# Optimization experiments

Measured on AMD Instinct MI355X. Metric: run time of the kernel, lower is better.

The kernel has to match this reference:

```python
import jax, jax.numpy as jnp
import numpy as np

DIM = 768
HEADS = 12
HEAD_DIM = DIM // HEADS
B, N = 8, 1024


def setup_inputs() -> dict:
    key = jax.random.key(0)
    ks = jax.random.split(key, 5)
    x = jax.random.normal(ks[0], (B, N, DIM), dtype=jnp.float32)
    shared_rel_pos = jax.random.normal(ks[1], (HEADS, N, N), dtype=jnp.float32)
    qkv_w = jax.random.normal(ks[2], (3 * DIM, DIM), dtype=jnp.float32) * (DIM ** -0.5)
    proj_w = jax.random.normal(ks[3], (DIM, DIM), dtype=jnp.float32) * (DIM ** -0.5)
    proj_b = jnp.zeros((DIM,), dtype=jnp.float32)
    return {"x": x, "shared_rel_pos": shared_rel_pos, "qkv_w": qkv_w,
            "proj_w": proj_w, "proj_b": proj_b}


def reference(x, shared_rel_pos, qkv_w, proj_w, proj_b):
    Bt, Nt, C = x.shape
    scale = HEAD_DIM ** -0.5
    # qkv: Linear(dim, 3*dim, bias=False) -> (B, N, 3, H, hd) -> (3, B, H, N, hd)
    qkv = jnp.einsum('bnc,oc->bno', x, qkv_w)
    qkv = qkv.reshape(Bt, Nt, 3, HEADS, HEAD_DIM).transpose(2, 0, 3, 1, 4)
    q, k, v = qkv[0], qkv[1], qkv[2]
    # scaled dot-product attention with shared relative-position bias
    attn = jnp.einsum('bhqd,bhkd->bhqk', q, k) * scale
    attn = attn + shared_rel_pos[None]  # broadcast over batch
    attn = jax.nn.softmax(attn, axis=-1)
    out = jnp.einsum('bhqk,bhkd->bhqd', attn, v)
    out = out.transpose(0, 2, 1, 3).reshape(Bt, Nt, C)
    return jnp.einsum('bnc,oc->bno', out, proj_w) + proj_b
```

## Files before the change

kernel.cpp:

```cpp
#include <hip/hip_runtime.h>
#include <hip/hip_bf16.h>
#include <stdint.h>

#define HEADS 12
#define HD 64
#define SEQ 1024
#define CDIM 768

typedef __attribute__((ext_vector_type(8))) short bfrag;
typedef __attribute__((ext_vector_type(4))) float facc;
typedef __attribute__((ext_vector_type(4))) _Float16 h4;

__device__ __forceinline__ ushort f2bf(float f) {
    union { float f; uint32_t u; } v; v.f = f;
    uint32_t u = v.u;
    uint32_t r = (u + 0x7FFFu + ((u >> 16) & 1u)) >> 16;
    return (ushort)r;
}
__device__ __forceinline__ ushort f2h(float f) {
    union { _Float16 h; ushort u; } c; c.h = (_Float16)f; return c.u;
}
__device__ __forceinline__ float h2f(uint32_t u16) {
    union { _Float16 h; ushort u; } c; c.u = (ushort)u16; return (float)c.h;
}

__global__ void cvt_all(const float* __restrict__ x, const float* __restrict__ qw,
                        const float* __restrict__ pw, const float* __restrict__ rel,
                        ushort* __restrict__ xd, ushort* __restrict__ qd,
                        ushort* __restrict__ pd, ushort* __restrict__ rd) {
    long i = ((long)blockIdx.x * 256 + threadIdx.x) * 4;
    if (i < 6291456) {
        float4 v = *(const float4*)(x + i);
        ushort4 o = {f2bf(v.x), f2bf(v.y), f2bf(v.z), f2bf(v.w)};
        *(ushort4*)(xd + i) = o;
    } else if (i < 8060928) {
        long j = i - 6291456;
        float4 v = *(const float4*)(qw + j);
        ushort4 o = {f2bf(v.x), f2bf(v.y), f2bf(v.z), f2bf(v.w)};
        *(ushort4*)(qd + j) = o;
    } else if (i < 8650752) {
        long j = i - 8060928;
        float4 v = *(const float4*)(pw + j);
        ushort4 o = {f2bf(v.x), f2bf(v.y), f2bf(v.z), f2bf(v.w)};
        *(ushort4*)(pd + j) = o;
    } else {
        long j = i - 8650752;
        float4 v = *(const float4*)(rel + j);
        ushort4 o = {f2h(v.x * 1.44269504f), f2h(v.y * 1.44269504f),
                     f2h(v.z * 1.44269504f), f2h(v.w * 1.44269504f)};
        *(ushort4*)(rd + j) = o;
    }
}

#define GLOAD16(gsrc, ldst) \
    __builtin_amdgcn_global_load_lds((const __attribute__((address_space(1))) uint32_t*)(gsrc), \
                                     (__attribute__((address_space(3))) uint32_t*)(ldst), 16, 0, 0)

template<int EPI>
__global__ __launch_bounds__(256) void gemm_nt(
    const ushort* __restrict__ A, const ushort* __restrict__ Bm,
    ushort* __restrict__ qb, ushort* __restrict__ kb, ushort* __restrict__ vb,
    const float* __restrict__ projb, float* __restrict__ out)
{
    __shared__ ushort As[128 * 32];
    __shared__ ushort Bs[128 * 32];
    const int t = threadIdx.x;
    const int w = t >> 6, l = t & 63;
    const int wm = w >> 1, wn = w & 1;
    const int lr = l & 15, lg = l >> 4;
    const int m0 = blockIdx.x * 128;
    const int o0 = blockIdx.y * 128;

    facc acc[4][4] = {};

    const int srow = w * 16 + (l >> 2);
    const int scol = (l & 3) * 8;
    const ushort* Ag = A + (size_t)(m0 + srow) * CDIM + scol;
    const ushort* Bg = Bm + (size_t)(o0 + srow) * CDIM + scol;

    for (int k0 = 0; k0 < CDIM; k0 += 32) {
        __syncthreads();
        GLOAD16(Ag + k0,             As + w * 512);
        GLOAD16(Ag + 64 * CDIM + k0, As + 2048 + w * 512);
        GLOAD16(Bg + k0,             Bs + w * 512);
        GLOAD16(Bg + 64 * CDIM + k0, Bs + 2048 + w * 512);
        __syncthreads();
        bfrag af[4], bf[4];
#pragma unroll
        for (int m = 0; m < 4; ++m)
            af[m] = *(const bfrag*)&As[(wm * 64 + m * 16 + lr) * 32 + lg * 8];
#pragma unroll
        for (int n = 0; n < 4; ++n)
            bf[n] = *(const bfrag*)&Bs[(wn * 64 + n * 16 + lr) * 32 + lg * 8];
#pragma unroll
        for (int m = 0; m < 4; ++m)
#pragma unroll
            for (int n = 0; n < 4; ++n)
                acc[m][n] = __builtin_amdgcn_mfma_f32_16x16x32_bf16(af[m], bf[n], acc[m][n], 0, 0, 0);
    }

    if (EPI == 0) {
        const int tsel = o0 / CDIM;
        const int h_base = (o0 % CDIM) / 64;
        ushort* dst = (tsel == 0) ? qb : ((tsel == 1) ? kb : vb);
        const float scl = (tsel == 0) ? 0.18033688f : 1.0f;
#pragma unroll
        for (int m = 0; m < 4; ++m) {
            int grow = m0 + wm * 64 + m * 16 + lg * 4;
#pragma unroll
            for (int n = 0; n < 4; ++n) {
                int h = h_base + wn;
                int d = n * 16 + lr;
#pragma unroll
                for (int r = 0; r < 4; ++r) {
                    int row = grow + r;
                    int b = row >> 10, nn = row & 1023;
                    ushort val = (tsel == 2) ? f2h(acc[m][n][r])
                                             : f2bf(acc[m][n][r] * scl);
                    dst[(((size_t)(b * HEADS + h)) * SEQ + nn) * HD + d] = val;
                }
            }
        }
    } else {
#pragma unroll
        for (int m = 0; m < 4; ++m) {
            int grow = m0 + wm * 64 + m * 16 + lg * 4;
#pragma unroll
            for (int n = 0; n < 4; ++n) {
                int o = o0 + wn * 64 + n * 16 + lr;
                float bias = projb[o];
#pragma unroll
                for (int r = 0; r < 4; ++r)
                    out[(size_t)(grow + r) * CDIM + o] = acc[m][n][r] + bias;
            }
        }
    }
}

__global__ __launch_bounds__(256, 4) void attn_kernel(
    const ushort* __restrict__ qbuf, const ushort* __restrict__ kbuf,
    const ushort* __restrict__ vbuf, const ushort* __restrict__ biash,
    ushort* __restrict__ attn_out)
{
    __shared__ ushort Ks[2][64 * 72];
    __shared__ ushort Vt[2][64 * 72];

    const int t = threadIdx.x;
    const int w = t >> 6, l = t & 63;
    const int lr = l & 15, lg = l >> 4;

    const int bid = blockIdx.x;
    const int lid = (bid & 7) * 192 + (bid >> 3);
    const int h  = lid >> 7;
    const int qt = (lid >> 3) & 15;
    const int b  = lid & 7;

    const int q0 = qt * 64;
    const size_t headoff = (size_t)(b * HEADS + h) * SEQ * HD;
    const int qrb = q0 + w * 16;

    bfrag aQ0, aQ1;
    {
        const ushort* Qp = qbuf + headoff + (size_t)(qrb + lr) * HD;
        aQ0 = *(const bfrag*)(Qp + lg * 8);
        aQ1 = *(const bfrag*)(Qp + 32 + lg * 8);
    }

    float mrun = -1e30f, lrun = 0.0f;
    facc Ov[4] = {};

    const ushort* bprow = biash + ((size_t)h * SEQ + qrb + lr) * SEQ;

    const int krow = t >> 3, kc = (t & 7) * 8;
    const int p2 = t & 31, vg_ = t >> 5;
    const ushort* kgb = kbuf + headoff + (size_t)krow * HD + kc;
    const ushort* vgb = vbuf + headoff + (size_t)(2 * p2) * HD + vg_ * 8;

    bfrag krA = *(const bfrag*)(kgb);
    bfrag krB = *(const bfrag*)(kgb + (size_t)32 * HD);
    bfrag vrA = *(const bfrag*)(vgb);
    bfrag vrB = *(const bfrag*)(vgb + HD);
    uint2 bcur[4], bnxt[4];
#pragma unroll
    for (int c = 0; c < 4; ++c)
        bcur[c] = *(const uint2*)(bprow + c * 16 + lg * 4);

    *(bfrag*)&Ks[0][krow * 72 + kc] = krA;
    *(bfrag*)&Ks[0][(krow + 32) * 72 + kc] = krB;
#pragma unroll
    for (int i = 0; i < 8; ++i) {
        uint32_t pk = (uint32_t)(uint16_t)vrA[i] | ((uint32_t)(uint16_t)vrB[i] << 16);
        *(uint32_t*)&Vt[0][(vg_ * 8 + i) * 72 + 2 * p2] = pk;
    }
    krA = *(const bfrag*)(kgb + (size_t)64 * HD);
    krB = *(const bfrag*)(kgb + (size_t)96 * HD);
    vrA = *(const bfrag*)(vgb + (size_t)64 * HD);
    vrB = *(const bfrag*)(vgb + (size_t)65 * HD);
    __syncthreads();

    for (int tt = 0; tt < 16; ++tt) {
        const int cur = tt & 1;
        const ushort* Kc = Ks[cur];
        const ushort* Vc = Vt[cur];

        facc St[4];
        h4 pf[4];
        float psum = 0.0f, pmax = -3.0e38f;
#pragma unroll
        for (int c = 0; c < 4; ++c) {
            bfrag kf0 = *(const bfrag*)&Kc[(c * 16 + lr) * 72 + lg * 8];
            bfrag kf1 = *(const bfrag*)&Kc[(c * 16 + lr) * 72 + 32 + lg * 8];
            uint2 bb = bcur[c];
            facc s;
            s[0] = h2f(bb.x & 0xffffu);
            s[1] = h2f(bb.x >> 16);
            s[2] = h2f(bb.y & 0xffffu);
            s[3] = h2f(bb.y >> 16);
            __builtin_amdgcn_s_setprio(1);
            s = __builtin_amdgcn_mfma_f32_16x16x32_bf16(kf0, aQ0, s, 0, 0, 0);
            s = __builtin_amdgcn_mfma_f32_16x16x32_bf16(kf1, aQ1, s, 0, 0, 0);
            __builtin_amdgcn_s_setprio(0);
            St[c] = s;
#pragma unroll
            for (int r = 0; r < 4; ++r) {
                float p = exp2f(s[r] - mrun);
                psum += p;
                pf[c][r] = (_Float16)p;
                pmax = fmaxf(pmax, s[r]);
            }
        }

        if (tt < 15) {
            const int kvn = (tt + 1) << 6;
#pragma unroll
            for (int c = 0; c < 4; ++c)
                bnxt[c] = *(const uint2*)(bprow + kvn + c * 16 + lg * 4);
        }

        pmax = fmaxf(pmax, __shfl_xor(pmax, 16));
        pmax = fmaxf(pmax, __shfl_xor(pmax, 32));
        if (!__all(pmax <= mrun + 11.541560f)) {
            float mnew = fmaxf(mrun, pmax);
            float al = exp2f(mrun - mnew);
            psum = 0.0f;
#pragma unroll
            for (int c = 0; c < 4; ++c)
#pragma unroll
                for (int r = 0; r < 4; ++r) {
                    float p = exp2f(St[c][r] - mnew);
                    psum += p;
                    pf[c][r] = (_Float16)p;
                }
#pragma unroll
            for (int r = 0; r < 4; ++r) {
                float a = __shfl(al, lg * 4 + r);
#pragma unroll
                for (int d = 0; d < 4; ++d) Ov[d][r] *= a;
            }
            lrun *= al;
            mrun = mnew;
        }
        psum += __shfl_xor(psum, 16);
        psum += __shfl_xor(psum, 32);
        lrun += psum;

        if (tt < 15) {
            *(bfrag*)&Ks[cur ^ 1][krow * 72 + kc] = krA;
            *(bfrag*)&Ks[cur ^ 1][(krow + 32) * 72 + kc] = krB;
#pragma unroll
            for (int i = 0; i < 8; ++i) {
                uint32_t pk = (uint32_t)(uint16_t)vrA[i] | ((uint32_t)(uint16_t)vrB[i] << 16);
                *(uint32_t*)&Vt[cur ^ 1][(vg_ * 8 + i) * 72 + 2 * p2] = pk;
            }
        }
        if (tt < 14) {
            const int kvn = (tt + 2) << 6;
            krA = *(const bfrag*)(kgb + (size_t)kvn * HD);
            krB = *(const bfrag*)(kgb + (size_t)(kvn + 32) * HD);
            vrA = *(const bfrag*)(vgb + (size_t)kvn * HD);
            vrB = *(const bfrag*)(vgb + (size_t)(kvn + 1) * HD);
        }

        __builtin_amdgcn_s_setprio(1);
#pragma unroll
        for (int d0 = 0; d0 < 4; ++d0) {
#pragma unroll
            for (int c = 0; c < 4; ++c) {
                h4 bv = *(const h4*)&Vc[(d0 * 16 + lr) * 72 + c * 16 + lg * 4];
                Ov[d0] = __builtin_amdgcn_mfma_f32_16x16x16f16(pf[c], bv, Ov[d0], 0, 0, 0);
            }
        }
        __builtin_amdgcn_s_setprio(0);

        if (tt < 15) {
            __syncthreads();
#pragma unroll
            for (int c = 0; c < 4; ++c)
                bcur[c] = bnxt[c];
        }
    }

    ushort* op = attn_out + ((size_t)b * SEQ + qrb) * CDIM + h * HD;
#pragma unroll
    for (int r = 0; r < 4; ++r) {
        float ll = __shfl(lrun, lg * 4 + r);
        float rl = 1.0f / ll;
#pragma unroll
        for (int d = 0; d < 4; ++d)
            op[(size_t)(lg * 4 + r) * CDIM + d * 16 + lr] = f2bf(Ov[d][r] * rl);
    }
}

extern "C" void kernel_launch(void* const* d_in, const int* in_sizes, int n_in,
                              void* d_out, int out_size, void* d_ws, size_t ws_size,
                              hipStream_t stream) {
    const float* x     = (const float*)d_in[0];
    const float* rel   = (const float*)d_in[1];
    const float* qkvw  = (const float*)d_in[2];
    const float* projw = (const float*)d_in[3];
    const float* projb = (const float*)d_in[4];
    float* out = (float*)d_out;

    char* ws = (char*)d_ws;
    ushort* biash = (ushort*)(ws);
    ushort* qb    = (ushort*)(ws + 25165824);
    ushort* kb    = (ushort*)(ws + 37748736);
    ushort* vb    = (ushort*)(ws + 50331648);
    ushort* attnb = (ushort*)(ws + 62914560);
    ushort* xbf   = attnb;
    ushort* wbf   = (ushort*)(ws + 75497472);
    ushort* pwbf  = (ushort*)(ws + 79036416);

    cvt_all<<<20736, 256, 0, stream>>>(x, qkvw, projw, rel, xbf, wbf, pwbf, biash);

    gemm_nt<0><<<dim3(64, 18), 256, 0, stream>>>(xbf, wbf, qb, kb, vb, nullptr, nullptr);
    attn_kernel<<<1536, 256, 0, stream>>>(qb, kb, vb, biash, attnb);
    gemm_nt<1><<<dim3(64, 6), 256, 0, stream>>>(attnb, pwbf, nullptr, nullptr, nullptr, projb, out);
}
```

Measured before the change: 164.0 us.

## Fuse bias conversion into QKV GEMM grid and widen attention blocks to 512 threads

Moves the fp32-to-fp16 conversion of the relative-position bias out of the standalone convert kernel and into extra blocks of the QKV GEMM launch, so it runs concurrently with the GEMM. Attention now uses 512-thread blocks covering 128 queries, so K/V tiles are shared by twice as many waves and each thread loads half as much K/V per tile. Softmax uses raw v_exp_f32, packed fp16 conversion with round-toward-zero, a looser rescale threshold checked via __any, and defers the cross-lane row-sum reduction to the end. These cut per-tile ALU, shuffle and load work, at the cost of higher register/LDS pressure per block and slightly different rounding.

```diff
diff --git a/kernel.cpp b/kernel.cpp
--- a/kernel.cpp
+++ b/kernel.cpp
@@ -6,10 +6,12 @@
 #define HD 64
 #define SEQ 1024
 #define CDIM 768
+#define LOG2E 1.44269504f
 
 typedef __attribute__((ext_vector_type(8))) short bfrag;
 typedef __attribute__((ext_vector_type(4))) float facc;
 typedef __attribute__((ext_vector_type(4))) _Float16 h4;
+typedef __attribute__((ext_vector_type(2))) __fp16 pk2;
 
 __device__ __forceinline__ ushort f2bf(float f) {
     union { float f; uint32_t u; } v; v.f = f;
@@ -23,11 +25,22 @@
 __device__ __forceinline__ float h2f(uint32_t u16) {
     union { _Float16 h; ushort u; } c; c.u = (ushort)u16; return (float)c.h;
 }
+__device__ __forceinline__ h4 pack4h(float p0, float p1, float p2, float p3) {
+    union { h4 v4; pk2 v2[2]; } u;
+    u.v2[0] = __builtin_amdgcn_cvt_pkrtz(p0, p1);
+    u.v2[1] = __builtin_amdgcn_cvt_pkrtz(p2, p3);
+    return u.v4;
+}
+__device__ __forceinline__ float exp2_raw(float x) {
+    float r;
+    asm("v_exp_f32 %0, %1" : "=v"(r) : "v"(x));
+    return r;
+}
 
 __global__ void cvt_all(const float* __restrict__ x, const float* __restrict__ qw,
-                        const float* __restrict__ pw, const float* __restrict__ rel,
+                        const float* __restrict__ pw,
                         ushort* __restrict__ xd, ushort* __restrict__ qd,
-                        ushort* __restrict__ pd, ushort* __restrict__ rd) {
+                        ushort* __restrict__ pd) {
     long i = ((long)blockIdx.x * 256 + threadIdx.x) * 4;
     if (i < 6291456) {
         float4 v = *(const float4*)(x + i);
@@ -43,12 +56,6 @@
         float4 v = *(const float4*)(pw + j);
         ushort4 o = {f2bf(v.x), f2bf(v.y), f2bf(v.z), f2bf(v.w)};
         *(ushort4*)(pd + j) = o;
-    } else {
-        long j = i - 8650752;
-        float4 v = *(const float4*)(rel + j);
-        ushort4 o = {f2h(v.x * 1.44269504f), f2h(v.y * 1.44269504f),
-                     f2h(v.z * 1.44269504f), f2h(v.w * 1.44269504f)};
-        *(ushort4*)(rd + j) = o;
     }
 }
 
@@ -60,11 +67,25 @@
 __global__ __launch_bounds__(256) void gemm_nt(
     const ushort* __restrict__ A, const ushort* __restrict__ Bm,
     ushort* __restrict__ qb, ushort* __restrict__ kb, ushort* __restrict__ vb,
-    const float* __restrict__ projb, float* __restrict__ out)
+    const float* __restrict__ projb, float* __restrict__ out,
+    const float* __restrict__ relf, ushort* __restrict__ biash)
 {
     __shared__ ushort As[128 * 32];
     __shared__ ushort Bs[128 * 32];
     const int t = threadIdx.x;
+
+    if (EPI == 0 && blockIdx.y >= 18) {
+        long cb = (long)(blockIdx.y - 18) * 64 + blockIdx.x;
+        long i = (cb * 256 + t) * 4;
+        if (i < 12582912) {
+            float4 v = *(const float4*)(relf + i);
+            ushort4 o = {f2h(v.x * LOG2E), f2h(v.y * LOG2E),
+                         f2h(v.z * LOG2E), f2h(v.w * LOG2E)};
+            *(ushort4*)(biash + i) = o;
+        }
+        return;
+    }
+
     const int w = t >> 6, l = t & 63;
     const int wm = w >> 1, wn = w & 1;
     const int lr = l & 15, lg = l >> 4;
@@ -137,7 +158,7 @@
     }
 }
 
-__global__ __launch_bounds__(256, 4) void attn_kernel(
+__global__ __launch_bounds__(512, 4) void attn_kernel(
     const ushort* __restrict__ qbuf, const ushort* __restrict__ kbuf,
     const ushort* __restrict__ vbuf, const ushort* __restrict__ biash,
     ushort* __restrict__ attn_out)
@@ -150,12 +171,12 @@
     const int lr = l & 15, lg = l >> 4;
 
     const int bid = blockIdx.x;
-    const int lid = (bid & 7) * 192 + (bid >> 3);
-    const int h  = lid >> 7;
-    const int qt = (lid >> 3) & 15;
+    const int lid = (bid & 7) * 96 + (bid >> 3);
+    const int h  = lid >> 6;
+    const int qt = (lid >> 3) & 7;
     const int b  = lid & 7;
 
-    const int q0 = qt * 64;
+    const int q0 = qt * 128;
     const size_t headoff = (size_t)(b * HEADS + h) * SEQ * HD;
     const int qrb = q0 + w * 16;
 
@@ -166,7 +187,8 @@
         aQ1 = *(const bfrag*)(Qp + 32 + lg * 8);
     }
 
-    float mrun = -1e30f, lrun = 0.0f;
+    float mrun = -1e30f;
+    float lrun = 0.0f;
     facc Ov[4] = {};
 
     const ushort* bprow = biash + ((size_t)h * SEQ + qrb + lr) * SEQ;
@@ -174,28 +196,25 @@
     const int krow = t >> 3, kc = (t & 7) * 8;
     const int p2 = t & 31, vg_ = t >> 5;
     const ushort* kgb = kbuf + headoff + (size_t)krow * HD + kc;
-    const ushort* vgb = vbuf + headoff + (size_t)(2 * p2) * HD + vg_ * 8;
+    const ushort* vgb = vbuf + headoff + (size_t)(2 * p2) * HD + vg_ * 4;
 
     bfrag krA = *(const bfrag*)(kgb);
-    bfrag krB = *(const bfrag*)(kgb + (size_t)32 * HD);
-    bfrag vrA = *(const bfrag*)(vgb);
-    bfrag vrB = *(const bfrag*)(vgb + HD);
-    uint2 bcur[4], bnxt[4];
+    ushort4 v0 = *(const ushort4*)(vgb);
+    ushort4 v1 = *(const ushort4*)(vgb + HD);
+    uint2 bcur[4];
 #pragma unroll
     for (int c = 0; c < 4; ++c)
         bcur[c] = *(const uint2*)(bprow + c * 16 + lg * 4);
 
     *(bfrag*)&Ks[0][krow * 72 + kc] = krA;
-    *(bfrag*)&Ks[0][(krow + 32) * 72 + kc] = krB;
-#pragma unroll
-    for (int i = 0; i < 8; ++i) {
-        uint32_t pk = (uint32_t)(uint16_t)vrA[i] | ((uint32_t)(uint16_t)vrB[i] << 16);
-        *(uint32_t*)&Vt[0][(vg_ * 8 + i) * 72 + 2 * p2] = pk;
+#pragma unroll
+    for (int i = 0; i < 4; ++i) {
+        uint32_t pk = (uint32_t)(&v0.x)[i] | ((uint32_t)(&v1.x)[i] << 16);
+        *(uint32_t*)&Vt[0][(vg_ * 4 + i) * 72 + 2 * p2] = pk;
     }
     krA = *(const bfrag*)(kgb + (size_t)64 * HD);
-    krB = *(const bfrag*)(kgb + (size_t)96 * HD);
-    vrA = *(const bfrag*)(vgb + (size_t)64 * HD);
-    vrB = *(const bfrag*)(vgb + (size_t)65 * HD);
+    v0 = *(const ushort4*)(vgb + (size_t)64 * HD);
+    v1 = *(const ushort4*)(vgb + (size_t)65 * HD);
     __syncthreads();
 
     for (int tt = 0; tt < 16; ++tt) {
@@ -221,36 +240,38 @@
             s = __builtin_amdgcn_mfma_f32_16x16x32_bf16(kf1, aQ1, s, 0, 0, 0);
             __builtin_amdgcn_s_setprio(0);
             St[c] = s;
-#pragma unroll
-            for (int r = 0; r < 4; ++r) {
-                float p = exp2f(s[r] - mrun);
-                psum += p;
-                pf[c][r] = (_Float16)p;
-                pmax = fmaxf(pmax, s[r]);
-            }
+            float p0 = exp2_raw(s[0] - mrun);
+            float p1 = exp2_raw(s[1] - mrun);
+            float p2f = exp2_raw(s[2] - mrun);
+            float p3 = exp2_raw(s[3] - mrun);
+            psum += (p0 + p1) + (p2f + p3);
+            pmax = fmaxf(pmax, fmaxf(fmaxf(s[0], s[1]), fmaxf(s[2], s[3])));
+            pf[c] = pack4h(p0, p1, p2f, p3);
         }
 
         if (tt < 15) {
             const int kvn = (tt + 1) << 6;
 #pragma unroll
             for (int c = 0; c < 4; ++c)
-                bnxt[c] = *(const uint2*)(bprow + kvn + c * 16 + lg * 4);
-        }
-
-        pmax = fmaxf(pmax, __shfl_xor(pmax, 16));
-        pmax = fmaxf(pmax, __shfl_xor(pmax, 32));
-        if (!__all(pmax <= mrun + 11.541560f)) {
-            float mnew = fmaxf(mrun, pmax);
-            float al = exp2f(mrun - mnew);
+                bcur[c] = *(const uint2*)(bprow + kvn + c * 16 + lg * 4);
+        }
+
+        if (__any(pmax > mrun + 14.0f)) {
+            float pm = pmax;
+            pm = fmaxf(pm, __shfl_xor(pm, 16));
+            pm = fmaxf(pm, __shfl_xor(pm, 32));
+            float mnew = fmaxf(mrun, pm);
+            float al = exp2_raw(mrun - mnew);
             psum = 0.0f;
 #pragma unroll
-            for (int c = 0; c < 4; ++c)
-#pragma unroll
-                for (int r = 0; r < 4; ++r) {
-                    float p = exp2f(St[c][r] - mnew);
-                    psum += p;
-                    pf[c][r] = (_Float16)p;
-                }
+            for (int c = 0; c < 4; ++c) {
+                float p0 = exp2_raw(St[c][0] - mnew);
+                float p1 = exp2_raw(St[c][1] - mnew);
+                float p2f = exp2_raw(St[c][2] - mnew);
+                float p3 = exp2_raw(St[c][3] - mnew);
+                psum += (p0 + p1) + (p2f + p3);
+                pf[c] = pack4h(p0, p1, p2f, p3);
+            }
 #pragma unroll
             for (int r = 0; r < 4; ++r) {
                 float a = __shfl(al, lg * 4 + r);
@@ -260,25 +281,21 @@
             lrun *= al;
             mrun = mnew;
         }
-        psum += __shfl_xor(psum, 16);
-        psum += __shfl_xor(psum, 32);
         lrun += psum;
 
         if (tt < 15) {
             *(bfrag*)&Ks[cur ^ 1][krow * 72 + kc] = krA;
-            *(bfrag*)&Ks[cur ^ 1][(krow + 32) * 72 + kc] = krB;
-#pragma unroll
-            for (int i = 0; i < 8; ++i) {
-                uint32_t pk = (uint32_t)(uint16_t)vrA[i] | ((uint32_t)(uint16_t)vrB[i] << 16);
-                *(uint32_t*)&Vt[cur ^ 1][(vg_ * 8 + i) * 72 + 2 * p2] = pk;
+#pragma unroll
+            for (int i = 0; i < 4; ++i) {
+                uint32_t pk = (uint32_t)(&v0.x)[i] | ((uint32_t)(&v1.x)[i] << 16);
+                *(uint32_t*)&Vt[cur ^ 1][(vg_ * 4 + i) * 72 + 2 * p2] = pk;
             }
         }
         if (tt < 14) {
-            const int kvn = (tt + 2) << 6;
-            krA = *(const bfrag*)(kgb + (size_t)kvn * HD);
-            krB = *(const bfrag*)(kgb + (size_t)(kvn + 32) * HD);
-            vrA = *(const bfrag*)(vgb + (size_t)kvn * HD);
-            vrB = *(const bfrag*)(vgb + (size_t)(kvn + 1) * HD);
+            const size_t kvn = (size_t)(tt + 2) << 6;
+            krA = *(const bfrag*)(kgb + kvn * HD);
+            v0 = *(const ushort4*)(vgb + kvn * HD);
+            v1 = *(const ushort4*)(vgb + (kvn + 1) * HD);
         }
 
         __builtin_amdgcn_s_setprio(1);
@@ -292,18 +309,16 @@
         }
         __builtin_amdgcn_s_setprio(0);
 
-        if (tt < 15) {
-            __syncthreads();
-#pragma unroll
-            for (int c = 0; c < 4; ++c)
-                bcur[c] = bnxt[c];
-        }
-    }
-
+        if (tt < 15) __syncthreads();
+    }
+
+    float lt = lrun;
+    lt += __shfl_xor(lt, 16);
+    lt += __shfl_xor(lt, 32);
     ushort* op = attn_out + ((size_t)b * SEQ + qrb) * CDIM + h * HD;
 #pragma unroll
     for (int r = 0; r < 4; ++r) {
-        float ll = __shfl(lrun, lg * 4 + r);
+        float ll = __shfl(lt, lg * 4 + r);
         float rl = 1.0f / ll;
 #pragma unroll
         for (int d = 0; d < 4; ++d)
@@ -331,9 +346,9 @@
     ushort* wbf   = (ushort*)(ws + 75497472);
     ushort* pwbf  = (ushort*)(ws + 79036416);
 
-    cvt_all<<<20736, 256, 0, stream>>>(x, qkvw, projw, rel, xbf, wbf, pwbf, biash);
-
-    gemm_nt<0><<<dim3(64, 18), 256, 0, stream>>>(xbf, wbf, qb, kb, vb, nullptr, nullptr);
-    attn_kernel<<<1536, 256, 0, stream>>>(qb, kb, vb, biash, attnb);
-    gemm_nt<1><<<dim3(64, 6), 256, 0, stream>>>(attnb, pwbf, nullptr, nullptr, nullptr, projb, out);
-}
+    cvt_all<<<8448, 256, 0, stream>>>(x, qkvw, projw, xbf, wbf, pwbf);
+
+    gemm_nt<0><<<dim3(64, 210), 256, 0, stream>>>(xbf, wbf, qb, kb, vb, nullptr, nullptr, rel, biash);
+    attn_kernel<<<768, 512, 0, stream>>>(qb, kb, vb, biash, attnb);
+    gemm_nt<1><<<dim3(64, 6), 256, 0, stream>>>(attnb, pwbf, nullptr, nullptr, nullptr, projb, out, nullptr, nullptr);
+}
```

New measurement: 167.2 us. No clear change (+1.9%).
